# Kernel tuning notes

Measured on AMD Instinct MI355X. Metric: run time of the kernel, lower is better.

The kernel has to match this reference:

```python
import jax, jax.numpy as jnp
import numpy as np

B, D, L, R, O = 32768, 128, 3, 64, 64
EPS = 1e-5


def setup_inputs() -> dict:
    key = jax.random.key(0)
    ks = jax.random.split(key, 5)
    s_in = 1.0 / np.sqrt(D)
    s_r = 1.0 / np.sqrt(R)
    return {
        "x": jax.random.normal(ks[0], (B, D, L), dtype=jnp.float32),
        "layer0": jax.random.uniform(ks[1], (D, R), minval=-s_in, maxval=s_in, dtype=jnp.float32),
        "core1": jax.random.uniform(ks[2], (R, D, R), minval=-s_in, maxval=s_in, dtype=jnp.float32),
        "core2": jax.random.uniform(ks[3], (R, D, R), minval=-s_in, maxval=s_in, dtype=jnp.float32),
        "last": jax.random.uniform(ks[4], (R, O), minval=-s_r, maxval=s_r, dtype=jnp.float32),
        "ln_w": jnp.ones((D, L), dtype=jnp.float32),
        "ln_b": jnp.zeros((D, L), dtype=jnp.float32),
    }


def reference(x, layer0, core1, core2, last, ln_w, ln_b):
    # LayerNorm over the last two dims [D, L] with affine params
    mu = jnp.mean(x, axis=(1, 2), keepdims=True)
    var = jnp.var(x, axis=(1, 2), keepdims=True)
    xn = (x - mu) * jax.lax.rsqrt(var + EPS) * ln_w + ln_b  # [B, D, L]

    # Tensor-train contraction chain. The original builds a khatri-rao
    # [B, R*D] per step then matmuls with the reshaped [R*D, R] core;
    # einsum 'br,bd,rds->bs' computes the identical contraction fused.
    temp = xn[:, :, 0] @ layer0  # [B, R]
    temp = jnp.einsum("br,bd,rds->bs", temp, xn[:, :, 1], core1)
    temp = jnp.einsum("br,bd,rds->bs", temp, xn[:, :, 2], core2)
    return temp @ last  # [B, O]
```

## Files before the change

### kernel.cpp

```cpp
#include <hip/hip_runtime.h>
#include <hip/hip_fp16.h>

typedef _Float16 f16x8 __attribute__((ext_vector_type(8)));
typedef float f32x16 __attribute__((ext_vector_type(16)));

union H2x4 { f16x8 v; __half2 h2[4]; unsigned u[4]; };
union U1H2 { unsigned u; __half2 h; };

#define TB 128
#define XN0_OFF  0
#define RING_OFF 32768
#define T_OFF    65536
#define XN12_OFF 81920
#define SMEM_BYTES 148480
#define WS_CT1   0
#define WS_CT2   1048576
#define WS_L0T   2097152
#define WS_LASTT 2113536

#define WAITBAR0() asm volatile("s_waitcnt vmcnt(0)\n\ts_barrier" ::: "memory")

__device__ __forceinline__ void gload_lds16(const void* g, void* l) {
  __builtin_amdgcn_global_load_lds(
      (const __attribute__((address_space(1))) unsigned int*)g,
      (__attribute__((address_space(3))) unsigned int*)l, 16, 0, 0);
}

__device__ __forceinline__ void issue_chunk16(const unsigned char* g,
                                              unsigned char* l, int tid) {
  gload_lds16(g + tid * 16, l + tid * 16);
  gload_lds16(g + tid * 16 + 8192, l + tid * 16 + 8192);
}

__device__ __forceinline__ unsigned pack_h2(float a, float b) {
  return (unsigned)__half_as_ushort(__float2half(a)) |
         ((unsigned)__half_as_ushort(__float2half(b)) << 16);
}

__device__ __forceinline__ void reduce_T(unsigned char* smem,
                                         f32x16 a0, f32x16 a1, f32x16 a2, f32x16 a3,
                                         int p, int kh, int h, int scol) {
  float* scr = (float*)(smem + (kh ? RING_OFF : XN0_OFF));
  __syncthreads();
  if (p == 0) {
#pragma unroll
    for (int j = 0; j < 16; ++j) {
      const int r0 = (j & 3) + 8 * (j >> 2) + 4 * h;
      scr[r0 * 64 + scol]        = a0[j];
      scr[(32 + r0) * 64 + scol] = a1[j];
      scr[(64 + r0) * 64 + scol] = a2[j];
      scr[(96 + r0) * 64 + scol] = a3[j];
    }
  }
  __syncthreads();
  if (p == 1) {
#pragma unroll
    for (int j = 0; j < 16; ++j) {
      const int r0 = (j & 3) + 8 * (j >> 2) + 4 * h;
      scr[r0 * 64 + scol]        += a0[j];
      scr[(32 + r0) * 64 + scol] += a1[j];
      scr[(64 + r0) * 64 + scol] += a2[j];
      scr[(96 + r0) * 64 + scol] += a3[j];
    }
  }
  __syncthreads();
  if (p == 0) {
    const float* s0 = (const float*)(smem + XN0_OFF);
    const float* s1 = (const float*)(smem + RING_OFF);
#pragma unroll
    for (int j = 0; j < 16; ++j) {
      const int r0 = (j & 3) + 8 * (j >> 2) + 4 * h;
      int row = kh * 32 + r0;
      float vsum = s0[row * 64 + scol] + s1[row * 64 + scol];
      *(__half*)(smem + T_OFF + row * 128 + ((2 * scol) ^ ((row & 7) << 4))) =
          __float2half(vsum);
      row += 64;
      vsum = s0[row * 64 + scol] + s1[row * 64 + scol];
      *(__half*)(smem + T_OFF + row * 128 + ((2 * scol) ^ ((row & 7) << 4))) =
          __float2half(vsum);
    }
  }
  __syncthreads();
}

__global__ void __launch_bounds__(512) tt_prep(
    const float* __restrict__ layer0, const float* __restrict__ core1,
    const float* __restrict__ core2, const float* __restrict__ last,
    unsigned char* __restrict__ ws) {
  const int tid = blockIdx.x * 512 + threadIdx.x;
  if (tid < 524288) {
    const int which = tid >> 18;
    const int w = tid & 262143;
    const float* core = which ? core2 : core1;
    unsigned char* ct = ws + (which ? WS_CT2 : WS_CT1);
    const int j   = w & 3;
    const int lp  = (w >> 2) & 63;
    const int blk = w >> 8;
    const int kbL = blk & 1;
    const int kh  = (blk >> 1) & 1;
    const int sb  = (blk >> 2) & 1;
    const int d   = blk >> 3;
    const int hh  = lp & 1;
    const int l31 = lp >> 1;
    const int s   = sb * 32 + l31;
    const int r0  = kh * 32 + kbL * 16 + hh * 8 + 2 * j;
    const unsigned val = pack_h2(core[r0 * 8192 + d * 64 + s],
                                 core[(r0 + 1) * 8192 + d * 64 + s]);
    *(unsigned*)(ct + (size_t)w * 4) = val;
  } else if (tid < 528384) {
    const int w = tid - 524288;
    const int r = w >> 6, j = w & 63, d = 2 * j;
    const unsigned val = pack_h2(layer0[d * 64 + r], layer0[(d + 1) * 64 + r]);
    *(unsigned*)(ws + WS_L0T + r * 256 + 4 * j) = val;
  } else if (tid < 530432) {
    const int w = tid - 528384;
    const int o = w >> 5, j = w & 31, r = 2 * j;
    const unsigned val = pack_h2(last[r * 64 + o], last[(r + 1) * 64 + o]);
    *(unsigned*)(ws + WS_LASTT + o * 128 + 4 * j) = val;
  }
}

#define KRSTEP(TPa, TPb, E, ACC)                                              \
  do {                                                                        \
    H2x4 af;                                                                  \
    _Pragma("unroll") for (int q = 0; q < 4; ++q)                             \
        af.h2[q] = __hmul2(TPa.h2[q], (E).h);                                 \
    ACC = __builtin_amdgcn_mfma_f32_32x32x16_f16(af.v, bf0, ACC, 0, 0, 0);    \
    _Pragma("unroll") for (int q = 0; q < 4; ++q)                             \
        af.h2[q] = __hmul2(TPb.h2[q], (E).h);                                 \
    ACC = __builtin_amdgcn_mfma_f32_32x32x16_f16(af.v, bf1, ACC, 0, 0, 0);    \
  } while (0)

__global__ void __launch_bounds__(512, 2) tt_fused(
    const float* __restrict__ x, const float* __restrict__ lnw,
    const float* __restrict__ lnb, const unsigned char* __restrict__ ws,
    float* __restrict__ out) {
  __shared__ alignas(16) unsigned char smem[SMEM_BYTES];
  const int tid = threadIdx.x;
  const int wid = tid >> 6;
  const int lane = tid & 63;
  const int l31 = lane & 31;
  const int h = lane >> 5;
  const int p  = wid & 1;
  const int kh = (wid >> 1) & 1;
  const int sb = (wid >> 2) & 1;
  const int bg0 = blockIdx.x * TB;
  const int scol = sb * 32 + l31;
  const int lp16 = (l31 * 2 + h) * 16;
  const int swzA = (l31 & 7) << 4;

  {
    float wv[6], bv[6];
#pragma unroll
    for (int k = 0; k < 6; ++k) { wv[k] = lnw[lane + 64 * k]; bv[k] = lnb[lane + 64 * k]; }
#pragma unroll
    for (int rr = 0; rr < 16; ++rr) {
      const int row = wid * 16 + rr;
      const float* xrow = x + (size_t)(bg0 + row) * 384;
      float v[6];
#pragma unroll
      for (int k = 0; k < 6; ++k) v[k] = xrow[lane + 64 * k];
      float s = 0.f, ss = 0.f;
#pragma unroll
      for (int k = 0; k < 6; ++k) { s += v[k]; ss += v[k] * v[k]; }
#pragma unroll
      for (int m = 1; m < 64; m <<= 1) { s += __shfl_xor(s, m); ss += __shfl_xor(ss, m); }
      const float mu = s * (1.f / 384.f);
      const float var = ss * (1.f / 384.f) - mu * mu;
      const float rstd = rsqrtf(var + 1e-5f);
#pragma unroll
      for (int k = 0; k < 6; ++k) {
        const int i = lane + 64 * k;
        const int d = i / 3;
        const int sl = i - 3 * d;
        const float xv = (v[k] - mu) * rstd * wv[k] + bv[k];
        if (sl == 0) {
          *(__half*)(smem + XN0_OFF + row * 256 + ((2 * d) ^ ((row & 7) << 4))) =
              __float2half(xv);
        } else {
          *(__half*)(smem + XN12_OFF + d * 520 + 4 * row + 2 * (sl - 1)) =
              __float2half(xv);
        }
      }
    }
  }
  __syncthreads();

  f32x16 acc0, acc1, acc2, acc3;

#pragma unroll
  for (int i = 0; i < 16; ++i) { acc0[i] = 0.f; acc1[i] = 0.f; acc2[i] = 0.f; acc3[i] = 0.f; }
  {
    const unsigned char* l0t = ws + WS_L0T;
#pragma unroll
    for (int kbL = 0; kbL < 2; ++kbL) {
      const int cb = (((p << 1) | kh) * 2 + kbL) * 32 + h * 16;
      f16x8 bf = *(const f16x8*)(l0t + scol * 256 + cb);
      f16x8 aA = *(const f16x8*)(smem + XN0_OFF + l31 * 256 + (cb ^ swzA));
      f16x8 aB = *(const f16x8*)(smem + XN0_OFF + (32 + l31) * 256 + (cb ^ swzA));
      f16x8 aC = *(const f16x8*)(smem + XN0_OFF + (64 + l31) * 256 + (cb ^ swzA));
      f16x8 aD = *(const f16x8*)(smem + XN0_OFF + (96 + l31) * 256 + (cb ^ swzA));
      acc0 = __builtin_amdgcn_mfma_f32_32x32x16_f16(aA, bf, acc0, 0, 0, 0);
      acc1 = __builtin_amdgcn_mfma_f32_32x32x16_f16(aB, bf, acc1, 0, 0, 0);
      acc2 = __builtin_amdgcn_mfma_f32_32x32x16_f16(aC, bf, acc2, 0, 0, 0);
      acc3 = __builtin_amdgcn_mfma_f32_32x32x16_f16(aD, bf, acc3, 0, 0, 0);
    }
  }
  reduce_T(smem, acc0, acc1, acc2, acc3, p, kh, h, scol);

  for (int st = 0; st < 2; ++st) {
    const unsigned char* ctg = ws + (st ? WS_CT2 : WS_CT1);

    issue_chunk16(ctg, smem + RING_OFF, tid);

    H2x4 tp00, tp01, tp10, tp11, tp20, tp21, tp30, tp31;
    {
      const int rb0 = kh * 64 + h * 16;
      tp00.v = *(const f16x8*)(smem + T_OFF + l31 * 128 + (rb0 ^ swzA));
      tp01.v = *(const f16x8*)(smem + T_OFF + l31 * 128 + ((rb0 + 32) ^ swzA));
      tp10.v = *(const f16x8*)(smem + T_OFF + (32 + l31) * 128 + (rb0 ^ swzA));
      tp11.v = *(const f16x8*)(smem + T_OFF + (32 + l31) * 128 + ((rb0 + 32) ^ swzA));
      tp20.v = *(const f16x8*)(smem + T_OFF + (64 + l31) * 128 + (rb0 ^ swzA));
      tp21.v = *(const f16x8*)(smem + T_OFF + (64 + l31) * 128 + ((rb0 + 32) ^ swzA));
      tp30.v = *(const f16x8*)(smem + T_OFF + (96 + l31) * 128 + (rb0 ^ swzA));
      tp31.v = *(const f16x8*)(smem + T_OFF + (96 + l31) * 128 + ((rb0 + 32) ^ swzA));
    }

#pragma unroll
    for (int i = 0; i < 16; ++i) { acc0[i] = 0.f; acc1[i] = 0.f; acc2[i] = 0.f; acc3[i] = 0.f; }

#pragma unroll 1
    for (int cg = 0; cg < 64; ++cg) {
      WAITBAR0();
      if (cg < 63)
        issue_chunk16(ctg + (cg + 1) * 16384,
                      smem + RING_OFF + ((cg + 1) & 1) * 16384, tid);
      const unsigned char* bp = smem + RING_OFF + (cg & 1) * 16384 +
                                p * 8192 + sb * 4096 + kh * 2048 + lp16;
      f16x8 bf0 = *(const f16x8*)(bp);
      f16x8 bf1 = *(const f16x8*)(bp + 1024);
      const unsigned char* xp = smem + XN12_OFF + (2 * cg + p) * 520 +
                                4 * l31 + 2 * st;
      const unsigned xv0 = *(const unsigned short*)(xp);
      const unsigned xv1 = *(const unsigned short*)(xp + 128);
      const unsigned xv2 = *(const unsigned short*)(xp + 256);
      const unsigned xv3 = *(const unsigned short*)(xp + 384);
      U1H2 e0, e1, e2, e3;
      e0.u = xv0 | (xv0 << 16);
      e1.u = xv1 | (xv1 << 16);
      e2.u = xv2 | (xv2 << 16);
      e3.u = xv3 | (xv3 << 16);
      KRSTEP(tp00, tp01, e0, acc0);
      KRSTEP(tp10, tp11, e1, acc1);
      KRSTEP(tp20, tp21, e2, acc2);
      KRSTEP(tp30, tp31, e3, acc3);
    }
    reduce_T(smem, acc0, acc1, acc2, acc3, p, kh, h, scol);
  }

  if (p == 0) {
    f32x16 accd0, accd1;
#pragma unroll
    for (int i = 0; i < 16; ++i) { accd0[i] = 0.f; accd1[i] = 0.f; }
    const unsigned char* lastT = ws + WS_LASTT;
#pragma unroll
    for (int kb = 0; kb < 4; ++kb) {
      const int cb = kb * 32 + h * 16;
      f16x8 bf = *(const f16x8*)(lastT + scol * 128 + cb);
      f16x8 af0 = *(const f16x8*)(smem + T_OFF + (kh * 32 + l31) * 128 + (cb ^ swzA));
      f16x8 af1 = *(const f16x8*)(smem + T_OFF + (64 + kh * 32 + l31) * 128 + (cb ^ swzA));
      accd0 = __builtin_amdgcn_mfma_f32_32x32x16_f16(af0, bf, accd0, 0, 0, 0);
      accd1 = __builtin_amdgcn_mfma_f32_32x32x16_f16(af1, bf, accd1, 0, 0, 0);
    }
#pragma unroll
    for (int j = 0; j < 16; ++j) {
      const int r0 = (j & 3) + 8 * (j >> 2) + 4 * h;
      out[(size_t)(bg0 + kh * 32 + r0) * 64 + scol] = accd0[j];
      out[(size_t)(bg0 + 64 + kh * 32 + r0) * 64 + scol] = accd1[j];
    }
  }
}

extern "C" void kernel_launch(void* const* d_in, const int* in_sizes, int n_in,
                              void* d_out, int out_size, void* d_ws, size_t ws_size,
                              hipStream_t stream) {
  const float* x      = (const float*)d_in[0];
  const float* layer0 = (const float*)d_in[1];
  const float* core1  = (const float*)d_in[2];
  const float* core2  = (const float*)d_in[3];
  const float* last   = (const float*)d_in[4];
  const float* lnw    = (const float*)d_in[5];
  const float* lnb    = (const float*)d_in[6];
  unsigned char* ws   = (unsigned char*)d_ws;
  float* outp         = (float*)d_out;

  tt_prep<<<1036, 512, 0, stream>>>(layer0, core1, core2, last, ws);
  tt_fused<<<256, 512, 0, stream>>>(x, lnw, lnb, ws, outp);
}
```

Before: 104.4 us.

## Use 1024-thread blocks with four-way K split in the TT contraction

Doubles the threads per block from 512 to 1024, splitting the core contraction's K dimension four ways instead of two. Each wave runs half as many chunk iterations, and chunks double to 32 KB per pipeline step. The cross-wave reduction becomes a serialized three-pass accumulation with extra barriers. The aim is more MFMA parallelism per block, since the old 148 KB LDS footprint likely allowed only one 512-thread block per CU anyway. The trade-off is more reduction and synchronisation overhead and higher register pressure under the 1024-thread launch bound.

```diff
diff --git a/kernel.cpp b/kernel.cpp
--- a/kernel.cpp
+++ b/kernel.cpp
@@ -8,10 +8,10 @@
 union U1H2 { unsigned u; __half2 h; };
 
 #define TB 128
-#define XN0_OFF  0
-#define RING_OFF 32768
-#define T_OFF    65536
-#define XN12_OFF 81920
+#define SLOT0_OFF 0
+#define SLOT1_OFF 32768
+#define T_OFF     65536
+#define XN12_OFF  81920
 #define SMEM_BYTES 148480
 #define WS_CT1   0
 #define WS_CT2   1048576
@@ -26,10 +26,10 @@
       (__attribute__((address_space(3))) unsigned int*)l, 16, 0, 0);
 }
 
-__device__ __forceinline__ void issue_chunk16(const unsigned char* g,
+__device__ __forceinline__ void issue_chunk32(const unsigned char* g,
                                               unsigned char* l, int tid) {
   gload_lds16(g + tid * 16, l + tid * 16);
-  gload_lds16(g + tid * 16 + 8192, l + tid * 16 + 8192);
+  gload_lds16(g + tid * 16 + 16384, l + tid * 16 + 16384);
 }
 
 __device__ __forceinline__ unsigned pack_h2(float a, float b) {
@@ -39,10 +39,11 @@
 
 __device__ __forceinline__ void reduce_T(unsigned char* smem,
                                          f32x16 a0, f32x16 a1, f32x16 a2, f32x16 a3,
-                                         int p, int kh, int h, int scol) {
-  float* scr = (float*)(smem + (kh ? RING_OFF : XN0_OFF));
-  __syncthreads();
-  if (p == 0) {
+                                         int g4, int g2, int sb, int h, int scol,
+                                         int lane) {
+  float* scr = (float*)(smem + (g2 ? SLOT1_OFF : SLOT0_OFF));
+  __syncthreads();
+  if (g4 == 0) {
 #pragma unroll
     for (int j = 0; j < 16; ++j) {
       const int r0 = (j & 3) + 8 * (j >> 2) + 4 * h;
@@ -53,30 +54,29 @@
     }
   }
   __syncthreads();
-  if (p == 1) {
+#pragma unroll 1
+  for (int pass = 1; pass < 4; ++pass) {
+    if (g4 == pass) {
+#pragma unroll
+      for (int j = 0; j < 16; ++j) {
+        const int r0 = (j & 3) + 8 * (j >> 2) + 4 * h;
+        scr[r0 * 64 + scol]        += a0[j];
+        scr[(32 + r0) * 64 + scol] += a1[j];
+        scr[(64 + r0) * 64 + scol] += a2[j];
+        scr[(96 + r0) * 64 + scol] += a3[j];
+      }
+    }
+    __syncthreads();
+  }
+  if (g4 < 2) {
+    const float* s0 = (const float*)(smem + SLOT0_OFF);
+    const float* s1 = (const float*)(smem + SLOT1_OFF);
+    const int w = g2 * 2 + sb;
 #pragma unroll
     for (int j = 0; j < 16; ++j) {
-      const int r0 = (j & 3) + 8 * (j >> 2) + 4 * h;
-      scr[r0 * 64 + scol]        += a0[j];
-      scr[(32 + r0) * 64 + scol] += a1[j];
-      scr[(64 + r0) * 64 + scol] += a2[j];
-      scr[(96 + r0) * 64 + scol] += a3[j];
-    }
-  }
-  __syncthreads();
-  if (p == 0) {
-    const float* s0 = (const float*)(smem + XN0_OFF);
-    const float* s1 = (const float*)(smem + RING_OFF);
-#pragma unroll
-    for (int j = 0; j < 16; ++j) {
-      const int r0 = (j & 3) + 8 * (j >> 2) + 4 * h;
-      int row = kh * 32 + r0;
-      float vsum = s0[row * 64 + scol] + s1[row * 64 + scol];
-      *(__half*)(smem + T_OFF + row * 128 + ((2 * scol) ^ ((row & 7) << 4))) =
-          __float2half(vsum);
-      row += 64;
-      vsum = s0[row * 64 + scol] + s1[row * 64 + scol];
-      *(__half*)(smem + T_OFF + row * 128 + ((2 * scol) ^ ((row & 7) << 4))) =
+      const int row = w * 32 + g4 * 16 + j;
+      const float vsum = s0[row * 64 + lane] + s1[row * 64 + lane];
+      *(__half*)(smem + T_OFF + row * 128 + ((2 * lane) ^ ((row & 7) << 4))) =
           __float2half(vsum);
     }
   }
@@ -131,7 +131,7 @@
     ACC = __builtin_amdgcn_mfma_f32_32x32x16_f16(af.v, bf1, ACC, 0, 0, 0);    \
   } while (0)
 
-__global__ void __launch_bounds__(512, 2) tt_fused(
+__global__ void __launch_bounds__(1024, 1) tt_fused(
     const float* __restrict__ x, const float* __restrict__ lnw,
     const float* __restrict__ lnb, const unsigned char* __restrict__ ws,
     float* __restrict__ out) {
@@ -141,9 +141,9 @@
   const int lane = tid & 63;
   const int l31 = lane & 31;
   const int h = lane >> 5;
-  const int p  = wid & 1;
-  const int kh = (wid >> 1) & 1;
-  const int sb = (wid >> 2) & 1;
+  const int g4 = wid & 3;
+  const int g2 = (wid >> 2) & 1;
+  const int sb = (wid >> 3) & 1;
   const int bg0 = blockIdx.x * TB;
   const int scol = sb * 32 + l31;
   const int lp16 = (l31 * 2 + h) * 16;
@@ -154,8 +154,8 @@
 #pragma unroll
     for (int k = 0; k < 6; ++k) { wv[k] = lnw[lane + 64 * k]; bv[k] = lnb[lane + 64 * k]; }
 #pragma unroll
-    for (int rr = 0; rr < 16; ++rr) {
-      const int row = wid * 16 + rr;
+    for (int rr = 0; rr < 8; ++rr) {
+      const int row = wid * 8 + rr;
       const float* xrow = x + (size_t)(bg0 + row) * 384;
       float v[6];
 #pragma unroll
@@ -175,7 +175,7 @@
         const int sl = i - 3 * d;
         const float xv = (v[k] - mu) * rstd * wv[k] + bv[k];
         if (sl == 0) {
-          *(__half*)(smem + XN0_OFF + row * 256 + ((2 * d) ^ ((row & 7) << 4))) =
+          *(__half*)(smem + SLOT0_OFF + row * 256 + ((2 * d) ^ ((row & 7) << 4))) =
               __float2half(xv);
         } else {
           *(__half*)(smem + XN12_OFF + d * 520 + 4 * row + 2 * (sl - 1)) =
@@ -192,30 +192,28 @@
   for (int i = 0; i < 16; ++i) { acc0[i] = 0.f; acc1[i] = 0.f; acc2[i] = 0.f; acc3[i] = 0.f; }
   {
     const unsigned char* l0t = ws + WS_L0T;
-#pragma unroll
-    for (int kbL = 0; kbL < 2; ++kbL) {
-      const int cb = (((p << 1) | kh) * 2 + kbL) * 32 + h * 16;
-      f16x8 bf = *(const f16x8*)(l0t + scol * 256 + cb);
-      f16x8 aA = *(const f16x8*)(smem + XN0_OFF + l31 * 256 + (cb ^ swzA));
-      f16x8 aB = *(const f16x8*)(smem + XN0_OFF + (32 + l31) * 256 + (cb ^ swzA));
-      f16x8 aC = *(const f16x8*)(smem + XN0_OFF + (64 + l31) * 256 + (cb ^ swzA));
-      f16x8 aD = *(const f16x8*)(smem + XN0_OFF + (96 + l31) * 256 + (cb ^ swzA));
-      acc0 = __builtin_amdgcn_mfma_f32_32x32x16_f16(aA, bf, acc0, 0, 0, 0);
-      acc1 = __builtin_amdgcn_mfma_f32_32x32x16_f16(aB, bf, acc1, 0, 0, 0);
-      acc2 = __builtin_amdgcn_mfma_f32_32x32x16_f16(aC, bf, acc2, 0, 0, 0);
-      acc3 = __builtin_amdgcn_mfma_f32_32x32x16_f16(aD, bf, acc3, 0, 0, 0);
-    }
-  }
-  reduce_T(smem, acc0, acc1, acc2, acc3, p, kh, h, scol);
+    const int kq = wid & 7;
+    const int cb = kq * 32 + h * 16;
+    f16x8 bf = *(const f16x8*)(l0t + scol * 256 + cb);
+    f16x8 aA = *(const f16x8*)(smem + SLOT0_OFF + l31 * 256 + (cb ^ swzA));
+    f16x8 aB = *(const f16x8*)(smem + SLOT0_OFF + (32 + l31) * 256 + (cb ^ swzA));
+    f16x8 aC = *(const f16x8*)(smem + SLOT0_OFF + (64 + l31) * 256 + (cb ^ swzA));
+    f16x8 aD = *(const f16x8*)(smem + SLOT0_OFF + (96 + l31) * 256 + (cb ^ swzA));
+    acc0 = __builtin_amdgcn_mfma_f32_32x32x16_f16(aA, bf, acc0, 0, 0, 0);
+    acc1 = __builtin_amdgcn_mfma_f32_32x32x16_f16(aB, bf, acc1, 0, 0, 0);
+    acc2 = __builtin_amdgcn_mfma_f32_32x32x16_f16(aC, bf, acc2, 0, 0, 0);
+    acc3 = __builtin_amdgcn_mfma_f32_32x32x16_f16(aD, bf, acc3, 0, 0, 0);
+  }
+  reduce_T(smem, acc0, acc1, acc2, acc3, g4, g2, sb, h, scol, lane);
 
   for (int st = 0; st < 2; ++st) {
     const unsigned char* ctg = ws + (st ? WS_CT2 : WS_CT1);
 
-    issue_chunk16(ctg, smem + RING_OFF, tid);
+    issue_chunk32(ctg, smem + SLOT0_OFF, tid);
 
     H2x4 tp00, tp01, tp10, tp11, tp20, tp21, tp30, tp31;
     {
-      const int rb0 = kh * 64 + h * 16;
+      const int rb0 = g2 * 64 + h * 16;
       tp00.v = *(const f16x8*)(smem + T_OFF + l31 * 128 + (rb0 ^ swzA));
       tp01.v = *(const f16x8*)(smem + T_OFF + l31 * 128 + ((rb0 + 32) ^ swzA));
       tp10.v = *(const f16x8*)(smem + T_OFF + (32 + l31) * 128 + (rb0 ^ swzA));
@@ -230,16 +228,16 @@
     for (int i = 0; i < 16; ++i) { acc0[i] = 0.f; acc1[i] = 0.f; acc2[i] = 0.f; acc3[i] = 0.f; }
 
 #pragma unroll 1
-    for (int cg = 0; cg < 64; ++cg) {
+    for (int cg = 0; cg < 32; ++cg) {
       WAITBAR0();
-      if (cg < 63)
-        issue_chunk16(ctg + (cg + 1) * 16384,
-                      smem + RING_OFF + ((cg + 1) & 1) * 16384, tid);
-      const unsigned char* bp = smem + RING_OFF + (cg & 1) * 16384 +
-                                p * 8192 + sb * 4096 + kh * 2048 + lp16;
+      if (cg < 31)
+        issue_chunk32(ctg + (cg + 1) * 32768,
+                      smem + ((cg + 1) & 1) * 32768, tid);
+      const unsigned char* bp = smem + (cg & 1) * 32768 +
+                                g4 * 8192 + sb * 4096 + g2 * 2048 + lp16;
       f16x8 bf0 = *(const f16x8*)(bp);
       f16x8 bf1 = *(const f16x8*)(bp + 1024);
-      const unsigned char* xp = smem + XN12_OFF + (2 * cg + p) * 520 +
+      const unsigned char* xp = smem + XN12_OFF + (4 * cg + g4) * 520 +
                                 4 * l31 + 2 * st;
       const unsigned xv0 = *(const unsigned short*)(xp);
       const unsigned xv1 = *(const unsigned short*)(xp + 128);
@@ -255,10 +253,10 @@
       KRSTEP(tp20, tp21, e2, acc2);
       KRSTEP(tp30, tp31, e3, acc3);
     }
-    reduce_T(smem, acc0, acc1, acc2, acc3, p, kh, h, scol);
-  }
-
-  if (p == 0) {
+    reduce_T(smem, acc0, acc1, acc2, acc3, g4, g2, sb, h, scol, lane);
+  }
+
+  if (g4 == 0) {
     f32x16 accd0, accd1;
 #pragma unroll
     for (int i = 0; i < 16; ++i) { accd0[i] = 0.f; accd1[i] = 0.f; }
@@ -267,16 +265,16 @@
     for (int kb = 0; kb < 4; ++kb) {
       const int cb = kb * 32 + h * 16;
       f16x8 bf = *(const f16x8*)(lastT + scol * 128 + cb);
-      f16x8 af0 = *(const f16x8*)(smem + T_OFF + (kh * 32 + l31) * 128 + (cb ^ swzA));
-      f16x8 af1 = *(const f16x8*)(smem + T_OFF + (64 + kh * 32 + l31) * 128 + (cb ^ swzA));
+      f16x8 af0 = *(const f16x8*)(smem + T_OFF + (g2 * 32 + l31) * 128 + (cb ^ swzA));
+      f16x8 af1 = *(const f16x8*)(smem + T_OFF + (64 + g2 * 32 + l31) * 128 + (cb ^ swzA));
       accd0 = __builtin_amdgcn_mfma_f32_32x32x16_f16(af0, bf, accd0, 0, 0, 0);
       accd1 = __builtin_amdgcn_mfma_f32_32x32x16_f16(af1, bf, accd1, 0, 0, 0);
     }
 #pragma unroll
     for (int j = 0; j < 16; ++j) {
       const int r0 = (j & 3) + 8 * (j >> 2) + 4 * h;
-      out[(size_t)(bg0 + kh * 32 + r0) * 64 + scol] = accd0[j];
-      out[(size_t)(bg0 + 64 + kh * 32 + r0) * 64 + scol] = accd1[j];
+      out[(size_t)(bg0 + g2 * 32 + r0) * 64 + scol] = accd0[j];
+      out[(size_t)(bg0 + 64 + g2 * 32 + r0) * 64 + scol] = accd1[j];
     }
   }
 }
@@ -295,5 +293,5 @@
   float* outp         = (float*)d_out;
 
   tt_prep<<<1036, 512, 0, stream>>>(layer0, core1, core2, last, ws);
-  tt_fused<<<256, 512, 0, stream>>>(x, lnw, lnb, ws, outp);
-}
+  tt_fused<<<256, 1024, 0, stream>>>(x, lnw, lnb, ws, outp);
+}
```

Result: slower. 124.4 us (+19.2%).
